# Kernel optimization log

Measured on AMD Instinct MI355X. Metric: run time of the kernel, lower is better.

The kernel has to match this reference:

```python
import jax, jax.numpy as jnp
import numpy as np

F = 32        # nFilters
OPS = 5       # numOfOps (len(ratio))
CIN = 32      # in_planes of each filter's conv
N, H, W = 16, 128, 128
EPS = 1e-5    # BatchNorm2d default eps
RATIO = [0.3125, 0.3125, 0.1875, 0.125, 0.0625]


def setup_inputs() -> dict:
    key = jax.random.key(0)
    k1, k2 = jax.random.split(key, 2)
    x = jax.random.normal(k1, (N, CIN, H, W), jnp.float32)
    # each filter holds OPS weight variants (one per quantization op); 1 output channel each
    W_all = jax.random.normal(k2, (F, OPS, CIN, 3, 3), jnp.float32) * 0.05
    gamma = jnp.ones((F,), jnp.float32)
    beta = jnp.zeros((F,), jnp.float32)
    # setFiltersRatio: assign op index i to int(ratio[i]*F) consecutive filters
    counts = [int(r * F) for r in RATIO]
    counts[-1] = F - sum(counts[:-1])
    op_idx = jnp.asarray(np.repeat(np.arange(OPS), counts), jnp.int32)  # [F]
    return {"x": x, "W_all": W_all, "gamma": gamma, "beta": beta, "op_idx": op_idx}


def reference(x, W_all, gamma, beta, op_idx):
    # per-filter selection of the active op's conv weight (irregular gather)
    Wsel = W_all[jnp.arange(W_all.shape[0]), op_idx]  # [F, CIN, 3, 3]
    # all per-filter 1-out-channel convs of the same x == one grouped conv to F channels
    out1 = jax.lax.conv_general_dilated(
        x, Wsel, window_strides=(1, 1), padding="SAME",
        dimension_numbers=("NCHW", "OIHW", "NCHW"))  # [N, F, H, W]
    # BatchNorm2d in training mode: batch statistics over (N, H, W) per channel
    mean = out1.mean(axis=(0, 2, 3), keepdims=True)
    var = ((out1 - mean) ** 2).mean(axis=(0, 2, 3), keepdims=True)
    out1 = (out1 - mean) * jax.lax.rsqrt(var + EPS)
    out1 = out1 * gamma[None, :, None, None] + beta[None, :, None, None]
    # op[1] per filter: (quantized) ReLU activation — same math for every op variant
    return jax.nn.relu(out1)
```

## Files before the change

kernel.cpp:

```cpp
#include <hip/hip_runtime.h>

#define NB   16
#define CINC 32
#define HH   128
#define WWD  128
#define FF   32
#define OPSN 5
#define EPSV 1e-5f

#define WS_WFRAG_BOFF   262400
#define WS_XT_BOFF      280832
#define WS_NEED         (280832 + (size_t)16*130*130*32*2)

typedef __attribute__((ext_vector_type(8))) short bf16x8;
typedef __attribute__((ext_vector_type(4))) float f32x4;

__device__ __forceinline__ unsigned short f2bf(float f) {
    unsigned u = __builtin_bit_cast(unsigned, f);
    u += 0x7FFFu + ((u >> 16) & 1u);
    return (unsigned short)(u >> 16);
}
__device__ __forceinline__ unsigned pack2(float lo, float hi) {
    return (unsigned)f2bf(lo) | ((unsigned)f2bf(hi) << 16);
}

__global__ __launch_bounds__(256) void transform_kernel(
    const float* __restrict__ x, const float* __restrict__ Wall,
    const int* __restrict__ opidx, unsigned short* __restrict__ xt,
    unsigned short* __restrict__ wfrag, float* __restrict__ acc)
{
    __shared__ float lds[128 * 35];
    const int bid = blockIdx.x;
    const int tid = threadIdx.x;

    if (bid == NB * 130) {
        for (int i = tid; i < 1024; i += 256) acc[i] = 0.f;
        for (int idx = tid; idx < 9216; idx += 256) {
            int frag = idx >> 9;
            int lane = (idx >> 3) & 63;
            int j    = idx & 7;
            int s = frag >> 1, m = frag & 1;
            int kh = s / 3, kw = s - 3 * kh;
            int f = m * 16 + (lane & 15);
            int c = ((lane >> 4) << 3) + j;
            float v = Wall[((size_t)(f * OPSN + opidx[f]) * 288) + c * 9 + kh * 3 + kw];
            wfrag[idx] = f2bf(v);
        }
        return;
    }

    const int idx = bid >> 3;
    const int n   = (bid & 7) * 2 + (idx / 130);
    const int hp  = idx % 130;

    unsigned short* rowp = xt + (size_t)(n * 130 + hp) * 130 * 32;
    uint4 zz = make_uint4(0, 0, 0, 0);

    if (hp == 0 || hp == 129) {
        for (int c = tid; c < 520; c += 256) ((uint4*)rowp)[c] = zz;
        return;
    }

    const int h = hp - 1;
    const float* xr = x + ((size_t)n * CINC * HH + h) * WWD;
    const int c  = tid >> 3;
    const int wq = tid & 7;
#pragma unroll
    for (int it = 0; it < 4; ++it) {
        int w4 = wq + it * 8;
        float4 v = ((const float4*)(xr + (size_t)c * (HH * WWD)))[w4];
        int w = w4 * 4;
        lds[(w + 0) * 35 + c] = v.x;
        lds[(w + 1) * 35 + c] = v.y;
        lds[(w + 2) * 35 + c] = v.z;
        lds[(w + 3) * 35 + c] = v.w;
    }
    __syncthreads();
    for (int cc = tid; cc < 512; cc += 256) {
        int p = cc >> 2, k = cc & 3;
        const float* s = &lds[p * 35 + k * 8];
        uint4 o;
        o.x = pack2(s[0], s[1]); o.y = pack2(s[2], s[3]);
        o.z = pack2(s[4], s[5]); o.w = pack2(s[6], s[7]);
        ((uint4*)rowp)[4 + cc] = o;
    }
    if (tid < 4)       ((uint4*)rowp)[tid] = zz;
    else if (tid < 8)  ((uint4*)rowp)[129 * 4 + tid - 4] = zz;
}

#define LOADROW(f0, f1, f2, R)                                                  \
    {                                                                           \
        const unsigned short* rp =                                              \
            xbase + ((size_t)(R) * 130 + w0) * 32 + laneoff;                    \
        f0 = *(const bf16x8*)(rp);                                              \
        f1 = *(const bf16x8*)(rp + 32);                                         \
        f2 = *(const bf16x8*)(rp + 64);                                         \
    }

#define MROW(f0, f1, f2, aA, aB, kh)                                            \
    {                                                                           \
        aA = __builtin_amdgcn_mfma_f32_16x16x32_bf16(wfr[2*((kh)*3+0)],   f0, aA, 0,0,0); \
        aB = __builtin_amdgcn_mfma_f32_16x16x32_bf16(wfr[2*((kh)*3+0)+1], f0, aB, 0,0,0); \
        aA = __builtin_amdgcn_mfma_f32_16x16x32_bf16(wfr[2*((kh)*3+1)],   f1, aA, 0,0,0); \
        aB = __builtin_amdgcn_mfma_f32_16x16x32_bf16(wfr[2*((kh)*3+1)+1], f1, aB, 0,0,0); \
        aA = __builtin_amdgcn_mfma_f32_16x16x32_bf16(wfr[2*((kh)*3+2)],   f2, aA, 0,0,0); \
        aB = __builtin_amdgcn_mfma_f32_16x16x32_bf16(wfr[2*((kh)*3+2)+1], f2, aB, 0,0,0); \
    }

#define CONV_TILE(FIN, H0, OBDECL)                                              \
    {                                                                           \
        OBDECL;                                                                 \
        f32x4 a0A = zz4, a0B = zz4, a1A = zz4, a1B = zz4;                       \
        f32x4 a2A = zz4, a2B = zz4, a3A = zz4, a3B = zz4;                       \
        bf16x8 c0, c1, c2, n0, n1, n2;                                          \
        LOADROW(c0, c1, c2, (H0));                                              \
        LOADROW(n0, n1, n2, (H0) + 1);                                          \
        MROW(c0, c1, c2, a0A, a0B, 0);                                          \
        LOADROW(c0, c1, c2, (H0) + 2);                                          \
        MROW(n0, n1, n2, a0A, a0B, 1);                                          \
        MROW(n0, n1, n2, a1A, a1B, 0);                                          \
        LOADROW(n0, n1, n2, (H0) + 3);                                          \
        MROW(c0, c1, c2, a0A, a0B, 2);                                          \
        MROW(c0, c1, c2, a1A, a1B, 1);                                          \
        MROW(c0, c1, c2, a2A, a2B, 0);                                          \
        FIN(a0A, a0B, 0);                                                       \
        LOADROW(c0, c1, c2, (H0) + 4);                                          \
        MROW(n0, n1, n2, a1A, a1B, 2);                                          \
        MROW(n0, n1, n2, a2A, a2B, 1);                                          \
        MROW(n0, n1, n2, a3A, a3B, 0);                                          \
        FIN(a1A, a1B, 1);                                                       \
        LOADROW(n0, n1, n2, (H0) + 5);                                          \
        MROW(c0, c1, c2, a2A, a2B, 2);                                          \
        MROW(c0, c1, c2, a3A, a3B, 1);                                          \
        FIN(a2A, a2B, 2);                                                       \
        MROW(n0, n1, n2, a3A, a3B, 2);                                          \
        FIN(a3A, a3B, 3);                                                       \
    }

#define NOOP_DECL (void)0

#define CONV_DECODE_512                                                         \
    const int bid  = blockIdx.x;                                                \
    const int tid  = threadIdx.x;                                               \
    const int n    = (bid & 7) * 2 + ((bid >> 3) & 1);                          \
    const int rest = bid >> 4;                                       \
    const int hbase= (rest & 15) * 8;                                           \
    const int wh   = rest >> 4;                                      \
    const int lane = tid & 63;                                                  \
    const int wv   = tid >> 6;                                                  \
    const int w0   = wh * 64 + wv * 16;                                         \
    const int l15  = lane & 15, lhi = lane >> 4;

#define WFR_LOAD                                                                \
    bf16x8 wfr[18];                                                             \
    _Pragma("unroll")                                                           \
    for (int i = 0; i < 18; ++i)                                                \
        wfr[i] = *(const bf16x8*)(wfrag + (i * 64 + lane) * 8);                 \
    const unsigned short* xbase = xt + (size_t)n * 130 * 130 * 32;              \
    const int laneoff = l15 * 32 + lhi * 8;                                     \
    f32x4 zz4 = {0.f, 0.f, 0.f, 0.f};

__global__ __launch_bounds__(256, 2) void conv_stats_kernel(
    const unsigned short* __restrict__ xt,
    const unsigned short* __restrict__ wfrag,
    float* __restrict__ acc)
{
    __shared__ float red[4][64];
    CONV_DECODE_512
    WFR_LOAD

    float s8[8], q8[8];
#pragma unroll
    for (int j = 0; j < 8; ++j) { s8[j] = 0.f; q8[j] = 0.f; }

#define FIN_STATS(aA, aB, hh)                                                   \
    {                                                                           \
        _Pragma("unroll")                                                       \
        for (int r = 0; r < 4; ++r) {                                           \
            float v0 = aA[r], v1 = aB[r];                                       \
            s8[r]     += v0;  q8[r]     += v0 * v0;                             \
            s8[4 + r] += v1;  q8[4 + r] += v1 * v1;                             \
        }                                                                       \
    }

    CONV_TILE(FIN_STATS, hbase,     NOOP_DECL)
    CONV_TILE(FIN_STATS, hbase + 4, NOOP_DECL)
#undef FIN_STATS

#pragma unroll
    for (int m = 1; m < 16; m <<= 1) {
#pragma unroll
        for (int j = 0; j < 8; ++j) {
            s8[j] += __shfl_xor(s8[j], m, 64);
            q8[j] += __shfl_xor(q8[j], m, 64);
        }
    }
    if (l15 == 0) {
#pragma unroll
        for (int j = 0; j < 8; ++j) {
            int f = (j < 4) ? (lhi * 4 + j) : (16 + lhi * 4 + (j - 4));
            red[wv][f]      = s8[j];
            red[wv][32 + f] = q8[j];
        }
    }
    __syncthreads();
    if (tid < 64) {
        float v = red[0][tid] + red[1][tid] + red[2][tid] + red[3][tid];
        atomicAdd(&acc[n * 64 + tid], v);
    }
}

__global__ __launch_bounds__(256, 2) void conv_apply_kernel(
    const unsigned short* __restrict__ xt,
    const unsigned short* __restrict__ wfrag,
    const float* __restrict__ acc,
    const float* __restrict__ gamma, const float* __restrict__ beta,
    float* __restrict__ out)
{
    __shared__ float tot[64];
    __shared__ float bns[64];
    CONV_DECODE_512

    if (tid < 64) {
        float s = 0.f;
#pragma unroll
        for (int k = 0; k < 16; ++k) s += acc[k * 64 + tid];
        tot[tid] = s;
    }
    __syncthreads();
    if (tid < 32) {
        float cnt  = (float)(NB * HH * WWD);
        float mean = tot[tid] / cnt;
        float var  = tot[32 + tid] / cnt - mean * mean;
        float sc   = gamma[tid] * rsqrtf(var + EPSV);
        bns[tid]      = sc;
        bns[32 + tid] = beta[tid] - mean * sc;
    }
    __syncthreads();

    WFR_LOAD

    float sc0[4], sh0[4], sc1[4], sh1[4];
#pragma unroll
    for (int r = 0; r < 4; ++r) {
        int f0 = lhi * 4 + r, f1 = 16 + lhi * 4 + r;
        sc0[r] = bns[f0]; sh0[r] = bns[32 + f0];
        sc1[r] = bns[f1]; sh1[r] = bns[32 + f1];
    }

#define FIN_APPLY(aA, aB, hh)                                                   \
    {                                                                           \
        _Pragma("unroll")                                                       \
        for (int r = 0; r < 4; ++r) {                                           \
            __builtin_nontemporal_store(                                        \
                fmaxf(fmaf(aA[r], sc0[r], sh0[r]), 0.f),                        \
                ob + (size_t)r * (HH * WWD) + (hh) * WWD);                      \
            __builtin_nontemporal_store(                                        \
                fmaxf(fmaf(aB[r], sc1[r], sh1[r]), 0.f),                        \
                ob + (size_t)r * (HH * WWD) + 16 * (HH * WWD) + (hh) * WWD);    \
        }                                                                       \
    }

    CONV_TILE(FIN_APPLY, hbase,
        float* ob = out + (size_t)(n * FF + lhi * 4) * (HH * WWD)
                        + hbase * WWD + w0 + l15)
    CONV_TILE(FIN_APPLY, hbase + 4,
        float* ob = out + (size_t)(n * FF + lhi * 4) * (HH * WWD)
                        + (hbase + 4) * WWD + w0 + l15)
#undef FIN_APPLY
}

__global__ __launch_bounds__(256) void conv_kernel(
    const float* __restrict__ x, const float* __restrict__ Wall,
    const int* __restrict__ opidx, float* __restrict__ out)
{
    __shared__ float wlds[FF * 289];
    __shared__ float xlds[8 * 3 * 132];
    const int tid = threadIdx.x;
    const int h = blockIdx.x;
    const int n = blockIdx.y;
    for (int i = tid; i < FF * 288; i += 256) {
        int f = i / 288;
        int r = i - f * 288;
        int op = opidx[f];
        wlds[f * 289 + r] = Wall[(f * OPSN + op) * 288 + r];
    }
    const int f = tid & 31;
    const int wg = tid >> 5;
    const int w0 = wg << 4;
    float acc[16];
#pragma unroll
    for (int i = 0; i < 16; ++i) acc[i] = 0.f;
    const float* xn = x + (size_t)n * CINC * HH * WWD;
    for (int cc = 0; cc < 4; ++cc) {
        __syncthreads();
        for (int i = tid; i < 8 * 3 * 132; i += 256) {
            int c8 = i / (3 * 132);
            int rem = i - c8 * (3 * 132);
            int r = rem / 132;
            int wp = rem - r * 132;
            int hin = h + r - 1;
            int win = wp - 1;
            float v = 0.f;
            if ((unsigned)hin < HH && (unsigned)win < WWD)
                v = xn[((cc * 8 + c8) * HH + hin) * WWD + win];
            xlds[i] = v;
        }
        __syncthreads();
#pragma unroll
        for (int c8 = 0; c8 < 8; ++c8) {
            const int c = cc * 8 + c8;
            float wv[9];
#pragma unroll
            for (int k = 0; k < 9; ++k) wv[k] = wlds[f * 289 + c * 9 + k];
#pragma unroll
            for (int kh = 0; kh < 3; ++kh) {
                float xr[20];
                const float4* p = (const float4*)&xlds[(c8 * 3 + kh) * 132 + w0];
#pragma unroll
                for (int j = 0; j < 5; ++j) {
                    float4 v = p[j];
                    xr[j * 4 + 0] = v.x; xr[j * 4 + 1] = v.y;
                    xr[j * 4 + 2] = v.z; xr[j * 4 + 3] = v.w;
                }
#pragma unroll
                for (int kw = 0; kw < 3; ++kw) {
                    float wgt = wv[kh * 3 + kw];
#pragma unroll
                    for (int i = 0; i < 16; ++i)
                        acc[i] = fmaf(xr[i + kw], wgt, acc[i]);
                }
            }
        }
    }
    float* op_ = out + (((size_t)(n * FF + f) * HH + h) * WWD + w0);
#pragma unroll
    for (int j = 0; j < 4; ++j)
        ((float4*)op_)[j] = make_float4(acc[j * 4], acc[j * 4 + 1],
                                        acc[j * 4 + 2], acc[j * 4 + 3]);
}

__global__ __launch_bounds__(256) void stats_kernel(
    const float* __restrict__ out, const float* __restrict__ gamma,
    const float* __restrict__ beta, float* __restrict__ ws)
{
    __shared__ float ssum[256], ssq[256];
    const int f = blockIdx.x;
    const int tid = threadIdx.x;
    float s = 0.f, q = 0.f;
    for (int n = 0; n < NB; ++n) {
        const float4* p = (const float4*)(out + (size_t)(n * FF + f) * HH * WWD);
        for (int i = tid; i < HH * WWD / 4; i += 256) {
            float4 v = p[i];
            s += v.x + v.y + v.z + v.w;
            q += v.x * v.x + v.y * v.y + v.z * v.z + v.w * v.w;
        }
    }
    ssum[tid] = s; ssq[tid] = q;
    __syncthreads();
    for (int st = 128; st > 0; st >>= 1) {
        if (tid < st) { ssum[tid] += ssum[tid + st]; ssq[tid] += ssq[tid + st]; }
        __syncthreads();
    }
    if (tid == 0) {
        float cnt = (float)(NB * HH * WWD);
        float mean = ssum[0] / cnt;
        float var = ssq[0] / cnt - mean * mean;
        float sc = gamma[f] * rsqrtf(var + EPSV);
        ws[f] = sc;
        ws[FF + f] = beta[f] - mean * sc;
    }
}

__global__ __launch_bounds__(256) void apply_kernel(
    float* __restrict__ out, const float* __restrict__ bnp)
{
    const int total4 = NB * FF * HH * WWD / 4;
    for (int i = blockIdx.x * 256 + threadIdx.x; i < total4; i += gridDim.x * 256) {
        int f = (i >> 12) & 31;
        float sc = bnp[f], sh = bnp[FF + f];
        float4 v = ((const float4*)out)[i];
        v.x = fmaxf(fmaf(v.x, sc, sh), 0.f);
        v.y = fmaxf(fmaf(v.y, sc, sh), 0.f);
        v.z = fmaxf(fmaf(v.z, sc, sh), 0.f);
        v.w = fmaxf(fmaf(v.w, sc, sh), 0.f);
        ((float4*)out)[i] = v;
    }
}

extern "C" void kernel_launch(void* const* d_in, const int* in_sizes, int n_in,
                              void* d_out, int out_size, void* d_ws, size_t ws_size,
                              hipStream_t stream) {
    const float* x     = (const float*)d_in[0];
    const float* Wall  = (const float*)d_in[1];
    const float* gamma = (const float*)d_in[2];
    const float* beta  = (const float*)d_in[3];
    const int*   opidx = (const int*)d_in[4];
    float* out = (float*)d_out;
    float* ws  = (float*)d_ws;

    if (ws_size >= WS_NEED) {
        float*          acc   = ws;
        unsigned short* wfrag = (unsigned short*)((char*)d_ws + WS_WFRAG_BOFF);
        unsigned short* xt    = (unsigned short*)((char*)d_ws + WS_XT_BOFF);

        transform_kernel<<<NB * 130 + 1, 256, 0, stream>>>(x, Wall, opidx, xt, wfrag, acc);
        conv_stats_kernel<<<512, 256, 0, stream>>>(xt, wfrag, acc);
        conv_apply_kernel<<<512, 256, 0, stream>>>(xt, wfrag, acc, gamma, beta, out);
    } else {
        dim3 gridc(HH, NB);
        conv_kernel<<<gridc, 256, 0, stream>>>(x, Wall, opidx, out);
        stats_kernel<<<FF, 256, 0, stream>>>(out, gamma, beta, ws);
        apply_kernel<<<2048, 256, 0, stream>>>(out, ws);
    }
}
```

Measured before the change: 39.09 us.

## Fuse conv-stats and apply kernels with grid-wide barrier, keep accumulators in registers

Merges the separate stats and apply passes into one persistent kernel. Conv results stay in registers (16 f32x4 accumulators), and a global atomic counter with a spin-wait acts as a grid barrier, so the last block computes the BN scale and shift and the others wait before applying them. This removes the second convolution recompute and one kernel launch. In exchange it raises register pressure and relies on all 512 blocks being co-resident; otherwise the spin-wait can deadlock.

```diff
diff --git a/kernel.cpp b/kernel.cpp
--- a/kernel.cpp
+++ b/kernel.cpp
@@ -8,6 +8,8 @@
 #define OPSN 5
 #define EPSV 1e-5f
 
+#define WS_CTL_BOFF     4096
+#define WS_BNP_BOFF     4160
 #define WS_WFRAG_BOFF   262400
 #define WS_XT_BOFF      280832
 #define WS_NEED         (280832 + (size_t)16*130*130*32*2)
@@ -27,7 +29,8 @@
 __global__ __launch_bounds__(256) void transform_kernel(
     const float* __restrict__ x, const float* __restrict__ Wall,
     const int* __restrict__ opidx, unsigned short* __restrict__ xt,
-    unsigned short* __restrict__ wfrag, float* __restrict__ acc)
+    unsigned short* __restrict__ wfrag, float* __restrict__ acc,
+    int* __restrict__ ctl)
 {
     __shared__ float lds[128 * 35];
     const int bid = blockIdx.x;
@@ -35,6 +38,7 @@
 
     if (bid == NB * 130) {
         for (int i = tid; i < 1024; i += 256) acc[i] = 0.f;
+        if (tid == 0) { ctl[0] = 0; ctl[1] = 0; }
         for (int idx = tid; idx < 9216; idx += 256) {
             int frag = idx >> 9;
             int lane = (idx >> 3) & 63;
@@ -107,37 +111,32 @@
         aB = __builtin_amdgcn_mfma_f32_16x16x32_bf16(wfr[2*((kh)*3+2)+1], f2, aB, 0,0,0); \
     }
 
-#define CONV_TILE(FIN, H0, OBDECL)                                              \
+#define CONV_TILE_KEEP(FIN, H0, A0, B0, A1, B1, A2, B2, A3, B3)                 \
     {                                                                           \
-        OBDECL;                                                                 \
-        f32x4 a0A = zz4, a0B = zz4, a1A = zz4, a1B = zz4;                       \
-        f32x4 a2A = zz4, a2B = zz4, a3A = zz4, a3B = zz4;                       \
         bf16x8 c0, c1, c2, n0, n1, n2;                                          \
         LOADROW(c0, c1, c2, (H0));                                              \
         LOADROW(n0, n1, n2, (H0) + 1);                                          \
-        MROW(c0, c1, c2, a0A, a0B, 0);                                          \
+        MROW(c0, c1, c2, A0, B0, 0);                                            \
         LOADROW(c0, c1, c2, (H0) + 2);                                          \
-        MROW(n0, n1, n2, a0A, a0B, 1);                                          \
-        MROW(n0, n1, n2, a1A, a1B, 0);                                          \
+        MROW(n0, n1, n2, A0, B0, 1);                                            \
+        MROW(n0, n1, n2, A1, B1, 0);                                            \
         LOADROW(n0, n1, n2, (H0) + 3);                                          \
-        MROW(c0, c1, c2, a0A, a0B, 2);                                          \
-        MROW(c0, c1, c2, a1A, a1B, 1);                                          \
-        MROW(c0, c1, c2, a2A, a2B, 0);                                          \
-        FIN(a0A, a0B, 0);                                                       \
+        MROW(c0, c1, c2, A0, B0, 2);                                            \
+        MROW(c0, c1, c2, A1, B1, 1);                                            \
+        MROW(c0, c1, c2, A2, B2, 0);                                            \
+        FIN(A0, B0);                                                            \
         LOADROW(c0, c1, c2, (H0) + 4);                                          \
-        MROW(n0, n1, n2, a1A, a1B, 2);                                          \
-        MROW(n0, n1, n2, a2A, a2B, 1);                                          \
-        MROW(n0, n1, n2, a3A, a3B, 0);                                          \
-        FIN(a1A, a1B, 1);                                                       \
+        MROW(n0, n1, n2, A1, B1, 2);                                            \
+        MROW(n0, n1, n2, A2, B2, 1);                                            \
+        MROW(n0, n1, n2, A3, B3, 0);                                            \
+        FIN(A1, B1);                                                            \
         LOADROW(n0, n1, n2, (H0) + 5);                                          \
-        MROW(c0, c1, c2, a2A, a2B, 2);                                          \
-        MROW(c0, c1, c2, a3A, a3B, 1);                                          \
-        FIN(a2A, a2B, 2);                                                       \
-        MROW(n0, n1, n2, a3A, a3B, 2);                                          \
-        FIN(a3A, a3B, 3);                                                       \
-    }
-
-#define NOOP_DECL (void)0
+        MROW(c0, c1, c2, A2, B2, 2);                                            \
+        MROW(c0, c1, c2, A3, B3, 1);                                            \
+        FIN(A2, B2);                                                            \
+        MROW(n0, n1, n2, A3, B3, 2);                                            \
+        FIN(A3, B3);                                                            \
+    }
 
 #define CONV_DECODE_512                                                         \
     const int bid  = blockIdx.x;                                                \
@@ -160,20 +159,30 @@
     const int laneoff = l15 * 32 + lhi * 8;                                     \
     f32x4 zz4 = {0.f, 0.f, 0.f, 0.f};
 
-__global__ __launch_bounds__(256, 2) void conv_stats_kernel(
+__global__ __launch_bounds__(256, 2) void fused_convbn_kernel(
     const unsigned short* __restrict__ xt,
     const unsigned short* __restrict__ wfrag,
-    float* __restrict__ acc)
+    float* __restrict__ acc, int* __restrict__ ctl,
+    float* __restrict__ bnp,
+    const float* __restrict__ gamma, const float* __restrict__ beta,
+    float* __restrict__ out)
 {
     __shared__ float red[4][64];
+    __shared__ float tot[64];
+    __shared__ float bns[64];
+    __shared__ int lastflag;
+
     CONV_DECODE_512
     WFR_LOAD
 
+    f32x4 u0A=zz4,u0B=zz4,u1A=zz4,u1B=zz4,u2A=zz4,u2B=zz4,u3A=zz4,u3B=zz4;
+    f32x4 v0A=zz4,v0B=zz4,v1A=zz4,v1B=zz4,v2A=zz4,v2B=zz4,v3A=zz4,v3B=zz4;
+
     float s8[8], q8[8];
 #pragma unroll
     for (int j = 0; j < 8; ++j) { s8[j] = 0.f; q8[j] = 0.f; }
 
-#define FIN_STATS(aA, aB, hh)                                                   \
+#define FIN_STATS(aA, aB)                                                       \
     {                                                                           \
         _Pragma("unroll")                                                       \
         for (int r = 0; r < 4; ++r) {                                           \
@@ -183,8 +192,8 @@
         }                                                                       \
     }
 
-    CONV_TILE(FIN_STATS, hbase,     NOOP_DECL)
-    CONV_TILE(FIN_STATS, hbase + 4, NOOP_DECL)
+    CONV_TILE_KEEP(FIN_STATS, hbase,     u0A,u0B,u1A,u1B,u2A,u2B,u3A,u3B)
+    CONV_TILE_KEEP(FIN_STATS, hbase + 4, v0A,v0B,v1A,v1B,v2A,v2B,v3A,v3B)
 #undef FIN_STATS
 
 #pragma unroll
@@ -208,37 +217,38 @@
         float v = red[0][tid] + red[1][tid] + red[2][tid] + red[3][tid];
         atomicAdd(&acc[n * 64 + tid], v);
     }
-}
-
-__global__ __launch_bounds__(256, 2) void conv_apply_kernel(
-    const unsigned short* __restrict__ xt,
-    const unsigned short* __restrict__ wfrag,
-    const float* __restrict__ acc,
-    const float* __restrict__ gamma, const float* __restrict__ beta,
-    float* __restrict__ out)
-{
-    __shared__ float tot[64];
-    __shared__ float bns[64];
-    CONV_DECODE_512
-
-    if (tid < 64) {
-        float s = 0.f;
-#pragma unroll
-        for (int k = 0; k < 16; ++k) s += acc[k * 64 + tid];
-        tot[tid] = s;
-    }
-    __syncthreads();
-    if (tid < 32) {
-        float cnt  = (float)(NB * HH * WWD);
-        float mean = tot[tid] / cnt;
-        float var  = tot[32 + tid] / cnt - mean * mean;
-        float sc   = gamma[tid] * rsqrtf(var + EPSV);
-        bns[tid]      = sc;
-        bns[32 + tid] = beta[tid] - mean * sc;
-    }
-    __syncthreads();
-
-    WFR_LOAD
+    __syncthreads();
+    if (tid == 0)
+        lastflag = (atomicAdd(&ctl[0], 1) == 511) ? 1 : 0;
+    __syncthreads();
+
+    if (lastflag) {
+        if (tid < 64) {
+            float s = 0.f;
+#pragma unroll
+            for (int k = 0; k < 16; ++k)
+                s += atomicAdd(&acc[k * 64 + tid], 0.f);
+            tot[tid] = s;
+        }
+        __syncthreads();
+        if (tid < 32) {
+            float cnt  = (float)(NB * HH * WWD);
+            float mean = tot[tid] / cnt;
+            float var  = tot[32 + tid] / cnt - mean * mean;
+            float sc   = gamma[tid] * rsqrtf(var + EPSV);
+            atomicExch(&bnp[tid], sc);
+            atomicExch(&bnp[FF + tid], beta[tid] - mean * sc);
+        }
+        __syncthreads();
+        if (tid == 0) atomicExch(&ctl[1], 1);
+    }
+
+    if (tid == 0) {
+        while (atomicAdd(&ctl[1], 0) == 0) __builtin_amdgcn_s_sleep(2);
+    }
+    __syncthreads();
+    if (tid < 64) bns[tid] = atomicAdd(&bnp[tid], 0.f);
+    __syncthreads();
 
     float sc0[4], sh0[4], sc1[4], sh1[4];
 #pragma unroll
@@ -261,12 +271,22 @@
         }                                                                       \
     }
 
-    CONV_TILE(FIN_APPLY, hbase,
+    {
         float* ob = out + (size_t)(n * FF + lhi * 4) * (HH * WWD)
-                        + hbase * WWD + w0 + l15)
-    CONV_TILE(FIN_APPLY, hbase + 4,
+                        + hbase * WWD + w0 + l15;
+        FIN_APPLY(u0A, u0B, 0);
+        FIN_APPLY(u1A, u1B, 1);
+        FIN_APPLY(u2A, u2B, 2);
+        FIN_APPLY(u3A, u3B, 3);
+    }
+    {
         float* ob = out + (size_t)(n * FF + lhi * 4) * (HH * WWD)
-                        + (hbase + 4) * WWD + w0 + l15)
+                        + (hbase + 4) * WWD + w0 + l15;
+        FIN_APPLY(v0A, v0B, 0);
+        FIN_APPLY(v1A, v1B, 1);
+        FIN_APPLY(v2A, v2B, 2);
+        FIN_APPLY(v3A, v3B, 3);
+    }
 #undef FIN_APPLY
 }
 
@@ -401,12 +421,15 @@
 
     if (ws_size >= WS_NEED) {
         float*          acc   = ws;
+        int*            ctl   = (int*)((char*)d_ws + WS_CTL_BOFF);
+        float*          bnp   = (float*)((char*)d_ws + WS_BNP_BOFF);
         unsigned short* wfrag = (unsigned short*)((char*)d_ws + WS_WFRAG_BOFF);
         unsigned short* xt    = (unsigned short*)((char*)d_ws + WS_XT_BOFF);
 
-        transform_kernel<<<NB * 130 + 1, 256, 0, stream>>>(x, Wall, opidx, xt, wfrag, acc);
-        conv_stats_kernel<<<512, 256, 0, stream>>>(xt, wfrag, acc);
-        conv_apply_kernel<<<512, 256, 0, stream>>>(xt, wfrag, acc, gamma, beta, out);
+        transform_kernel<<<NB * 130 + 1, 256, 0, stream>>>(x, Wall, opidx, xt,
+                                                           wfrag, acc, ctl);
+        fused_convbn_kernel<<<512, 256, 0, stream>>>(xt, wfrag, acc, ctl, bnp,
+                                                     gamma, beta, out);
     } else {
         dim3 gridc(HH, NB);
         conv_kernel<<<gridc, 256, 0, stream>>>(x, Wall, opidx, out);
```

New measurement: 53.83 us. 1.38x slower.
